# Kernel optimization log

Measured on AMD Instinct MI355X. Metric: run time of the kernel, lower is better.

The kernel has to match this reference:

```python
import jax, jax.numpy as jnp
import numpy as np

LRELU_SLOPE = 0.2
SQRT2 = 1.4142135623730951

def make_coord(h, w):
    # LIIF make_coord: cell-center coords in [-1, 1]; index 0 is the row (dim -2) coord.
    ys = -1.0 + (2.0 * jnp.arange(h, dtype=jnp.float32) + 1.0) / h
    xs = -1.0 + (2.0 * jnp.arange(w, dtype=jnp.float32) + 1.0) / w
    yy, xx = jnp.meshgrid(ys, xs, indexing='ij')
    return jnp.stack([yy, xx], axis=-1).reshape(h * w, 2)  # [Q, 2]

def style_layer(x, style_vec, scale2, shift, mod_w, mod_b, conv_w, act_b):
    # StyleGAN2-style modulated 3x3 conv + instance norm + (scale2, shift) affine + fused leaky relu.
    s = style_vec @ mod_w.T + mod_b                                   # [B, Cin] modulation
    w = conv_w[None] * s[:, None, :, None, None]                      # [B, Cout, Cin, 3, 3]
    demod = jax.lax.rsqrt(jnp.sum(w * w, axis=(2, 3, 4)) + 1e-8)      # [B, Cout]
    y = jax.lax.conv_general_dilated(x * s[:, :, None, None], conv_w, (1, 1), 'SAME',
                                     dimension_numbers=('NCHW', 'OIHW', 'NCHW'))
    y = y * demod[:, :, None, None]
    mu = jnp.mean(y, axis=(2, 3), keepdims=True)
    var = jnp.var(y, axis=(2, 3), keepdims=True)
    y = (y - mu) * jax.lax.rsqrt(var + 1e-5)                          # InstanceNorm2d (no affine)
    y = y * scale2 + shift
    return jax.nn.leaky_relu(y + act_b[None, :, None, None], LRELU_SLOPE) * SQRT2

def reference(x, scale1, scale2, shift, mod_w, mod_b, conv_w, act_b, w1, b1, w2, b2, out_h, out_w):
    B, C, Hf, Wf = x.shape
    feat = style_layer(x, scale1, scale2, shift, mod_w, mod_b, conv_w, act_b)
    Q = out_h * out_w
    coord = jnp.broadcast_to(make_coord(out_h, out_w)[None], (B, Q, 2))  # [B, Q, 2]
    rx = 1.0 / Hf  # = 2/Hf/2
    ry = 1.0 / Wf
    eps_shift = 1e-6
    feat_flat = feat.reshape(B, C, Hf * Wf).transpose(0, 2, 1)  # [B, Hf*Wf, C]
    preds, areas = [], []
    for vx in (-1, 1):
        for vy in (-1, 1):
            cy = jnp.clip(coord[..., 0] + vx * rx + eps_shift, -1.0 + 1e-6, 1.0 - 1e-6)
            cx = jnp.clip(coord[..., 1] + vy * ry + eps_shift, -1.0 + 1e-6, 1.0 - 1e-6)
            # nearest grid_sample (align_corners=False): idx = floor((c+1)/2 * size)
            iy = jnp.clip(jnp.floor((cy + 1.0) * 0.5 * Hf), 0, Hf - 1).astype(jnp.int32)
            ix = jnp.clip(jnp.floor((cx + 1.0) * 0.5 * Wf), 0, Wf - 1).astype(jnp.int32)
            lin = iy * Wf + ix                                        # [B, Q]
            q_feat = jnp.take_along_axis(feat_flat, lin[..., None], axis=1)  # [B, Q, C]
            qy = -1.0 + (2.0 * iy.astype(jnp.float32) + 1.0) / Hf     # nearest feat-cell coord
            qx = -1.0 + (2.0 * ix.astype(jnp.float32) + 1.0) / Wf
            rel_y = (coord[..., 0] - qy) * Hf
            rel_x = (coord[..., 1] - qx) * Wf
            inp = jnp.concatenate([q_feat, rel_y[..., None], rel_x[..., None]], axis=-1)  # [B,Q,C+2]
            pred = (inp @ w1 + b1) @ w2 + b2                          # two stacked Linears, no act
            preds.append(pred)
            areas.append(jnp.abs(rel_y * rel_x) + 1e-9)
    tot_area = areas[0] + areas[1] + areas[2] + areas[3]
    areas = [areas[3], areas[2], areas[1], areas[0]]  # diagonal swap (local ensemble)
    ret = jnp.zeros_like(preds[0])
    for pred, area in zip(preds, areas):
        ret = ret + pred * (area / tot_area)[..., None]
    return ret  # [B, Q, dim]

def setup_inputs() -> dict:
    key = jax.random.key(0)
    ks = jax.random.split(key, 12)
    B, C, Hf, Wf, S = 4, 64, 64, 64, 512
    return {
        'x': jax.random.normal(ks[0], (B, C, Hf, Wf), jnp.float32),
        'scale1': jax.random.normal(ks[1], (B, S), jnp.float32),
        'scale2': jax.random.normal(ks[2], (B, C, 1, 1), jnp.float32),
        'shift': jax.random.normal(ks[3], (B, C, 1, 1), jnp.float32),
        'mod_w': jax.random.normal(ks[4], (C, S), jnp.float32) * 0.02,
        'mod_b': jnp.ones((C,), jnp.float32),
        'conv_w': jax.random.normal(ks[5], (C, C, 3, 3), jnp.float32) * 0.05,
        'act_b': jax.random.normal(ks[6], (C,), jnp.float32) * 0.02,
        'w1': jax.random.normal(ks[7], (C + 2, 256), jnp.float32) * 0.05,
        'b1': jax.random.normal(ks[8], (256,), jnp.float32) * 0.01,
        'w2': jax.random.normal(ks[9], (256, C), jnp.float32) * 0.05,
        'b2': jax.random.normal(ks[10], (C,), jnp.float32) * 0.01,
        'out_h': 256,
        'out_w': 256,
    }
```

## Files before the change

kernel.cpp:

```cpp
#include <hip/hip_runtime.h>

#define SQRT2F 1.41421356237309515f

typedef __attribute__((ext_vector_type(8))) short bf16x8;
typedef __attribute__((ext_vector_type(4))) float f32x4;

enum : int {
  DM_OFF   = 0,
  BC_OFF   = 256,
  WC_OFF   = 1024,
  P_OFF    = 8192,
  Y_OFF    = 65536,
  WS_FLOATS = Y_OFF + 1048576
};

__device__ __align__(16) float WS[WS_FLOATS];
__device__ __align__(256) unsigned bar_cnt[4 * 64];
__device__ __align__(256) unsigned bar_gen[4 * 64];

__device__ __forceinline__ unsigned ld_llcu(const unsigned* p) {
  unsigned v;
  asm volatile("global_load_dword %0, %1, off sc0 sc1\n\ts_waitcnt vmcnt(0)"
               : "=v"(v) : "v"(p) : "memory");
  return v;
}
__device__ __forceinline__ float ld_llcf(const float* p) {
  float v;
  asm volatile("global_load_dword %0, %1, off sc0 sc1\n\ts_waitcnt vmcnt(0)"
               : "=v"(v) : "v"(p) : "memory");
  return v;
}
__device__ __forceinline__ f32x4 ld_llc4(const float* p) {
  f32x4 v;
  asm volatile("global_load_dwordx4 %0, %1, off sc0 sc1\n\ts_waitcnt vmcnt(0)"
               : "=v"(v) : "v"(p) : "memory");
  return v;
}
__device__ __forceinline__ void stg_llc1(float* p, float v) {
  asm volatile("global_store_dword %0, %1, off sc0 sc1"
               :: "v"(p), "v"(v) : "memory");
}
__device__ __forceinline__ void stg_llc4(float* p, f32x4 v) {
  asm volatile("global_store_dwordx4 %0, %1, off sc0 sc1"
               :: "v"(p), "v"(v) : "memory");
}

struct ConvSh {
  unsigned short Xl[3 * 66 * 64];
  unsigned short Wl[64 * 24 * 8];
  float part[512];
  float s_sh[64];
};
struct GoutSh {
  unsigned short ftb[128][72];
  unsigned short WcTb[64][72];
  float G[100][68];
  float red[2048];
  float A[64], B[64], bcl[64];
};
union ShU { ConvSh c; GoutSh g; };

__device__ __forceinline__ unsigned short f2bf(float v) {
  unsigned int u = __float_as_uint(v);
  u += 0x7fffu + ((u >> 16) & 1u);
  return (unsigned short)(u >> 16);
}

__global__ __launch_bounds__(512) void mega_kernel(
    const float* __restrict__ x,      const float* __restrict__ scale1,
    const float* __restrict__ scale2, const float* __restrict__ shiftp,
    const float* __restrict__ mod_w,  const float* __restrict__ mod_b,
    const float* __restrict__ conv_w, const float* __restrict__ act_b,
    const float* __restrict__ b1,     const float* __restrict__ w2,
    const float* __restrict__ b2,     const float* __restrict__ w1,
    float* __restrict__ out) {
  const int bid = blockIdx.x;
  const int b = bid >> 6;
  const int r = bid & 63;
  const int t = threadIdx.x;
  const int w = t >> 6, lane = t & 63;
  const int l15 = lane & 15, l4 = lane >> 4;

  __shared__ __align__(16) ShU sh;

  {
    const int i = t >> 3, qq = t & 7;
    const float* sv = scale1 + b * 512 + qq * 64;
    const float* mw = mod_w + i * 512 + qq * 64;
    float p = 0.f;
    for (int k = 0; k < 64; ++k) p = fmaf(sv[k], mw[k], p);
    sh.c.part[t] = p;
  }
  __syncthreads();
  if ((t & 7) == 0) {
    const int i = t >> 3;
    float s = mod_b[i];
    #pragma unroll
    for (int k = 0; k < 8; ++k) s += sh.c.part[t + k];
    sh.c.s_sh[i] = s;
  }
  __syncthreads();

  if (r == 0) {
    const int o = t >> 3, qq = t & 7;
    const float* cw = conv_w + o * 576 + qq * 72;
    float d = 0.f;
    #pragma unroll
    for (int ii = 0; ii < 8; ++ii) {
      const float ss = sh.c.s_sh[qq * 8 + ii];
      float wsq = 0.f;
      #pragma unroll
      for (int k = 0; k < 9; ++k) { const float wv = cw[ii * 9 + k]; wsq += wv * wv; }
      d += ss * ss * wsq;
    }
    sh.c.part[t] = d;
    __syncthreads();
    if ((t & 7) == 0) {
      float dd = 1e-8f;
      #pragma unroll
      for (int k = 0; k < 8; ++k) dd += sh.c.part[t + k];
      stg_llc1(&WS[DM_OFF + b * 64 + (t >> 3)], rsqrtf(dd));
    }
    __syncthreads();
  }

  if (r >= 1 && r <= 8) {
    const int idx = (r - 1) * 512 + t;
    const int c = idx >> 6, o = idx & 63;
    const float* r1 = w1 + c * 256;
    float a = 0.f;
    for (int k = 0; k < 256; ++k) a = fmaf(r1[k], w2[k * 64 + o], a);
    stg_llc1(&WS[WC_OFF + idx], a);
  } else if (r == 9) {
    if (t < 128) {
      const int idx = 4096 + t;
      const int c = idx >> 6, o = idx & 63;
      const float* r1 = w1 + c * 256;
      float a = 0.f;
      for (int k = 0; k < 256; ++k) a = fmaf(r1[k], w2[k * 64 + o], a);
      stg_llc1(&WS[WC_OFF + idx], a);
    } else if (t < 192) {
      const int o = t - 128;
      float a = 0.f;
      for (int k = 0; k < 256; ++k) a = fmaf(b1[k], w2[k * 64 + o], a);
      stg_llc1(&WS[BC_OFF + o], a + b2[o]);
    }
  }

  {
    int4* Xz = (int4*)sh.c.Xl;
    int4 z; z.x = z.y = z.z = z.w = 0;
    for (int idx = t; idx < 1584; idx += 512) Xz[idx] = z;
  }
  __syncthreads();

  {
    const int col = t & 63;
    const int tq = t >> 6;
    unsigned int* Xw = (unsigned int*)sh.c.Xl;
    #pragma unroll
    for (int it = 0; it < 12; ++it) {
      const int task = it * 8 + tq;
      const int row3 = task >> 5;
      const int ich = (task & 31) * 2;
      const int rr = r - 1 + row3;
      if (rr >= 0 && rr < 64) {
        const float* xb = x + ((size_t)(b * 64 + ich) << 12) + (rr << 6) + col;
        const float v0 = xb[0] * sh.c.s_sh[ich];
        const float v1 = xb[4096] * sh.c.s_sh[ich + 1];
        const unsigned int u = (unsigned int)f2bf(v0) | ((unsigned int)f2bf(v1) << 16);
        const int colp = col + 1;
        const int byte = ((row3 * 66 + colp) << 7) + ((((ich >> 3)) ^ (colp & 7)) << 4) + ((ich & 7) << 1);
        Xw[byte >> 2] = u;
      }
    }
  }

  const int oh = w >> 2, pg = w & 3;
  f32x4 acc[2];
  acc[0] = (f32x4){0.f, 0.f, 0.f, 0.f};
  acc[1] = (f32x4){0.f, 0.f, 0.f, 0.f};

  const bf16x8* Xv = (const bf16x8*)sh.c.Xl;
  const bf16x8* Wv = (const bf16x8*)sh.c.Wl;
  int4* Wst = (int4*)sh.c.Wl;

  for (int dy = 0; dy < 3; ++dy) {
    __syncthreads();
    #pragma unroll
    for (int i = 0; i < 3; ++i) {
      const int idx = i * 512 + t;
      const int o = idx / 24;
      const int g = idx - o * 24;
      const int dx = g >> 3, gg = g & 7;
      const float* cw = conv_w + o * 576 + (gg * 8) * 9 + dy * 3 + dx;
      int4 v;
      v.x = (int)((unsigned int)f2bf(cw[0])  | ((unsigned int)f2bf(cw[9])  << 16));
      v.y = (int)((unsigned int)f2bf(cw[18]) | ((unsigned int)f2bf(cw[27]) << 16));
      v.z = (int)((unsigned int)f2bf(cw[36]) | ((unsigned int)f2bf(cw[45]) << 16));
      v.w = (int)((unsigned int)f2bf(cw[54]) | ((unsigned int)f2bf(cw[63]) << 16));
      Wst[o * 24 + dx * 8 + (gg ^ (o & 7))] = v;
    }
    __syncthreads();

    #pragma unroll
    for (int dx = 0; dx < 3; ++dx) {
      #pragma unroll
      for (int kh = 0; kh < 2; ++kh) {
        const int kg = kh * 4 + l4;
        bf16x8 afr[2];
        #pragma unroll
        for (int m = 0; m < 2; ++m) {
          const int o = oh * 32 + m * 16 + l15;
          afr[m] = Wv[o * 24 + dx * 8 + (kg ^ (o & 7))];
        }
        const int colp = pg * 16 + l15 + dx;
        const bf16x8 bfr = Xv[((dy * 66 + colp) << 3) + (kg ^ (colp & 7))];
        #pragma unroll
        for (int m = 0; m < 2; ++m)
          acc[m] = __builtin_amdgcn_mfma_f32_16x16x32_bf16(
              afr[m], bfr, acc[m], 0, 0, 0);
      }
    }
  }

  {
    const int px = pg * 16 + l15;
    float* yq = WS + Y_OFF + (((size_t)b * 4096 + r * 64 + px) << 6);
    #pragma unroll
    for (int m = 0; m < 2; ++m)
      stg_llc4(yq + oh * 32 + m * 16 + l4 * 4, acc[m]);
  }

  __syncthreads();
  {
    float* sred = sh.c.part;
    #pragma unroll
    for (int m = 0; m < 2; ++m) {
      #pragma unroll
      for (int j = 0; j < 4; ++j) {
        float s1 = acc[m][j];
        float s2 = acc[m][j] * acc[m][j];
        #pragma unroll
        for (int off = 1; off < 16; off <<= 1) {
          s1 += __shfl_xor(s1, off);
          s2 += __shfl_xor(s2, off);
        }
        if (l15 == 0) {
          const int ol = m * 16 + l4 * 4 + j;
          sred[(w * 32 + ol) * 2 + 0] = s1;
          sred[(w * 32 + ol) * 2 + 1] = s2;
        }
      }
    }
    __syncthreads();
    if (t < 128) {
      const int o = t >> 1, wh = t & 1;
      const int ohh = o >> 5, ol = o & 31;
      float s = 0.f;
      #pragma unroll
      for (int pq = 0; pq < 4; ++pq)
        s += sred[(((ohh * 4 + pq) * 32) + ol) * 2 + wh];
      stg_llc1(&WS[P_OFF + (((size_t)b * 64 + r) * 64 + o) * 2 + wh], s);
    }
  }

  asm volatile("s_waitcnt vmcnt(0)" ::: "memory");
  __syncthreads();
  if (t == 0) {
    unsigned* cnt = &bar_cnt[b * 64];
    unsigned* gen = &bar_gen[b * 64];
    const unsigned g0 = ld_llcu(gen);
    const unsigned old = __hip_atomic_fetch_add(cnt, 1u, __ATOMIC_RELAXED,
                                                __HIP_MEMORY_SCOPE_AGENT);
    if (old == 63u) {
      __hip_atomic_store(cnt, 0u, __ATOMIC_RELAXED, __HIP_MEMORY_SCOPE_AGENT);
      __hip_atomic_fetch_add(gen, 1u, __ATOMIC_RELAXED,
                             __HIP_MEMORY_SCOPE_AGENT);
    } else {
      while (ld_llcu(gen) == g0) __builtin_amdgcn_s_sleep(8);
    }
  }
  __syncthreads();

  const int ty = (bid >> 3) & 7;
  const int tx = bid & 7;
  float* WcL = &sh.g.G[0][0];

  {
    f32x4 ps = (f32x4){0.f, 0.f, 0.f, 0.f};
    const float* Pb = WS + P_OFF + (size_t)b * 8192;
    #pragma unroll
    for (int k = 0; k < 4; ++k) {
      const f32x4 v = ld_llc4(Pb + (size_t)(t + k * 512) * 4);
      ps += v;
    }
    *(f32x4*)&sh.g.red[(t >> 5) * 128 + (t & 31) * 4] = ps;

    for (int i4 = t; i4 < 1072; i4 += 512) {
      const f32x4 v = (i4 < 1056) ? ld_llc4(WS + WC_OFF + i4 * 4)
                                  : ld_llc4(WS + BC_OFF + (i4 - 1056) * 4);
      *(f32x4*)&WcL[i4 * 4] = v;
    }
  }
  __syncthreads();

  const int sub = t & 3, chb = sub * 16;
  float4 wa[4], wb[4];
  #pragma unroll
  for (int k = 0; k < 4; ++k) {
    wa[k] = *(const float4*)&WcL[64 * 64 + chb + k * 4];
    wb[k] = *(const float4*)&WcL[65 * 64 + chb + k * 4];
  }
  if (t < 64) {
    float S1 = 0.f, S2 = 0.f;
    #pragma unroll
    for (int m = 0; m < 16; ++m) {
      S1 += sh.g.red[m * 128 + t * 2];
      S2 += sh.g.red[m * 128 + t * 2 + 1];
    }
    const float mu = S1 * (1.f / 4096.f);
    const float var = S2 * (1.f / 4096.f) - mu * mu;
    const float dm = ld_llcf(WS + DM_OFF + b * 64 + t);
    const float rstd = rsqrtf(dm * dm * var + 1e-5f);
    const float A = dm * rstd * scale2[b * 64 + t];
    sh.g.A[t] = A;
    sh.g.B[t] = -mu * A + shiftp[b * 64 + t] + act_b[t];
    sh.g.bcl[t] = WcL[4224 + t];
  }
  {
    const int o = t >> 3, g = t & 7;
    int4 pk;
    unsigned int e0, e1, e2, e3;
    e0 = (unsigned int)f2bf(WcL[(g * 8 + 0) * 64 + o]) |
         ((unsigned int)f2bf(WcL[(g * 8 + 1) * 64 + o]) << 16);
    e1 = (unsigned int)f2bf(WcL[(g * 8 + 2) * 64 + o]) |
         ((unsigned int)f2bf(WcL[(g * 8 + 3) * 64 + o]) << 16);
    e2 = (unsigned int)f2bf(WcL[(g * 8 + 4) * 64 + o]) |
         ((unsigned int)f2bf(WcL[(g * 8 + 5) * 64 + o]) << 16);
    e3 = (unsigned int)f2bf(WcL[(g * 8 + 6) * 64 + o]) |
         ((unsigned int)f2bf(WcL[(g * 8 + 7) * 64 + o]) << 16);
    pk.x = (int)e0; pk.y = (int)e1; pk.z = (int)e2; pk.w = (int)e3;
    *(int4*)&sh.g.WcTb[o][g * 8] = pk;
  }
  __syncthreads();

  const int cy_base = ty * 8 - 1, cx_base = tx * 8 - 1;
  {
    const float4* A4 = (const float4*)sh.g.A;
    const float4* B4 = (const float4*)sh.g.B;
    const float* yb = WS + Y_OFF + ((size_t)b << 18);
    for (int f = t; f < 1600; f += 512) {
      const int cell = f >> 4, cq = f & 15;
      const int li = cell / 10, lj = cell - li * 10;
      const int ciy = cy_base + li, cix = cx_base + lj;
      if (ciy >= 0 && ciy < 64 && cix >= 0 && cix < 64) {
        const f32x4 y4 = ld_llc4(yb + (((size_t)(ciy << 6) + cix) << 6) + cq * 4);
        const float4 Av = A4[cq], Bv = B4[cq];
        float f0, f1, f2, f3, u;
        u = y4[0] * Av.x + Bv.x; f0 = (u > 0.f ? u : 0.2f * u) * SQRT2F;
        u = y4[1] * Av.y + Bv.y; f1 = (u > 0.f ? u : 0.2f * u) * SQRT2F;
        u = y4[2] * Av.z + Bv.z; f2 = (u > 0.f ? u : 0.2f * u) * SQRT2F;
        u = y4[3] * Av.w + Bv.w; f3 = (u > 0.f ? u : 0.2f * u) * SQRT2F;
        uint2 u2;
        u2.x = (unsigned int)f2bf(f0) | ((unsigned int)f2bf(f1) << 16);
        u2.y = (unsigned int)f2bf(f2) | ((unsigned int)f2bf(f3) << 16);
        *(uint2*)&sh.g.ftb[cell][cq * 4] = u2;
      }
    }
  }
  __syncthreads();

  if (w < 7) {
    bf16x8 afr[2];
    #pragma unroll
    for (int kt = 0; kt < 2; ++kt)
      afr[kt] = *(const bf16x8*)&sh.g.ftb[w * 16 + l15][kt * 32 + l4 * 8];
    #pragma unroll
    for (int n = 0; n < 4; ++n) {
      const float bcv = sh.g.bcl[n * 16 + l15];
      f32x4 gacc = (f32x4){bcv, bcv, bcv, bcv};
      #pragma unroll
      for (int kt = 0; kt < 2; ++kt) {
        const bf16x8 bfr =
            *(const bf16x8*)&sh.g.WcTb[n * 16 + l15][kt * 32 + l4 * 8];
        gacc = __builtin_amdgcn_mfma_f32_16x16x32_bf16(afr[kt], bfr, gacc, 0, 0, 0);
      }
      #pragma unroll
      for (int j = 0; j < 4; ++j) {
        const int row = w * 16 + l4 * 4 + j;
        if (row < 100) sh.g.G[row][n * 16 + l15] = gacc[j];
      }
    }
  }
  __syncthreads();

  const float lo = -1.f + 1e-6f, hi = 1.f - 1e-6f;
  #pragma unroll 1
  for (int pass = 0; pass < 8; ++pass) {
    const int qi = pass * 128 + (t >> 2);
    const int oy = (ty << 5) + (qi >> 5), ox = (tx << 5) + (qi & 31);

    const float cy0 = -1.f + (2.f * oy + 1.f) * (1.f / 256.f);
    const float cx0 = -1.f + (2.f * ox + 1.f) * (1.f / 256.f);

    int lcell[4];
    float area[4], rely[4], relx[4];
    int j = 0;
    #pragma unroll
    for (int vx = -1; vx <= 1; vx += 2) {
      #pragma unroll
      for (int vy = -1; vy <= 1; vy += 2) {
        float cy = cy0 + (float)vx * (1.f / 64.f) + 1e-6f;
        cy = fminf(fmaxf(cy, lo), hi);
        float cx = cx0 + (float)vy * (1.f / 64.f) + 1e-6f;
        cx = fminf(fmaxf(cx, lo), hi);
        const float fy = floorf((cy + 1.f) * 32.f);
        const float fx = floorf((cx + 1.f) * 32.f);
        const int iy = (int)fminf(fmaxf(fy, 0.f), 63.f);
        const int ix = (int)fminf(fmaxf(fx, 0.f), 63.f);
        const float qy = -1.f + (2.f * iy + 1.f) * (1.f / 64.f);
        const float qx = -1.f + (2.f * ix + 1.f) * (1.f / 64.f);
        const float ry_ = (cy0 - qy) * 64.f;
        const float rx_ = (cx0 - qx) * 64.f;
        lcell[j] = (iy - cy_base) * 10 + (ix - cx_base);
        rely[j] = ry_; relx[j] = rx_;
        area[j] = fabsf(ry_ * rx_) + 1e-9f;
        ++j;
      }
    }
    const float tot = area[0] + area[1] + area[2] + area[3];
    float wgt[4];
    #pragma unroll
    for (int k = 0; k < 4; ++k) wgt[k] = area[3 - k] / tot;
    const float swy = wgt[0] * rely[0] + wgt[1] * rely[1] + wgt[2] * rely[2] + wgt[3] * rely[3];
    const float swx = wgt[0] * relx[0] + wgt[1] * relx[1] + wgt[2] * relx[2] + wgt[3] * relx[3];

    float4 rr[4];
    #pragma unroll
    for (int k = 0; k < 4; ++k) {
      rr[k].x = swy * wa[k].x + swx * wb[k].x;
      rr[k].y = swy * wa[k].y + swx * wb[k].y;
      rr[k].z = swy * wa[k].z + swx * wb[k].z;
      rr[k].w = swy * wa[k].w + swx * wb[k].w;
    }
    #pragma unroll
    for (int jj = 0; jj < 4; ++jj) {
      const float4* gp = (const float4*)&sh.g.G[lcell[jj]][chb];
      const float wv = wgt[jj];
      #pragma unroll
      for (int k = 0; k < 4; ++k) {
        const float4 gv = gp[k];
        rr[k].x += wv * gv.x; rr[k].y += wv * gv.y;
        rr[k].z += wv * gv.z; rr[k].w += wv * gv.w;
      }
    }
    const size_t gq = ((size_t)b << 16) + (oy << 8) + ox;
    float4* op = (float4*)(out + (gq << 6) + chb);
    #pragma unroll
    for (int k = 0; k < 4; ++k) op[k] = rr[k];
  }
}

extern "C" void kernel_launch(void* const* d_in, const int* in_sizes, int n_in,
                              void* d_out, int out_size, void* d_ws, size_t ws_size,
                              hipStream_t stream) {
  (void)in_sizes; (void)n_in; (void)out_size; (void)d_ws; (void)ws_size;
  const float* x      = (const float*)d_in[0];
  const float* scale1 = (const float*)d_in[1];
  const float* scale2 = (const float*)d_in[2];
  const float* shiftp = (const float*)d_in[3];
  const float* mod_w  = (const float*)d_in[4];
  const float* mod_b  = (const float*)d_in[5];
  const float* conv_w = (const float*)d_in[6];
  const float* act_b  = (const float*)d_in[7];
  const float* w1     = (const float*)d_in[8];
  const float* b1     = (const float*)d_in[9];
  const float* w2     = (const float*)d_in[10];
  const float* b2     = (const float*)d_in[11];
  float* out = (float*)d_out;

  hipLaunchKernelGGL(mega_kernel, dim3(256), dim3(512), 0, stream,
                     x, scale1, scale2, shiftp, mod_w, mod_b, conv_w, act_b,
                     b1, w2, b2, w1, out);
}
```

Before: 64.42 us.

## Spread weight-fold work across all blocks, batch LLC loads, use single grid barrier

Precomputing the folded MLP weight matrix (w1·w2 and b1·w2+b2) was done by eight or nine blocks with 512 threads each. It now runs on 17 threads in each of the 256 blocks after the conv, which shortens the critical path in those blocks. The per-batch barrier becomes one global barrier over all 256 blocks, since every block now needs weights that other blocks produce. After the barrier, the partial-stat, weight and feature-tile loads are all issued before a single vmcnt wait instead of waiting after each load, at the cost of more registers. The global barrier adds contention on one counter and couples all batches.

```diff
diff --git a/kernel.cpp b/kernel.cpp
--- a/kernel.cpp
+++ b/kernel.cpp
@@ -15,8 +15,8 @@
 };
 
 __device__ __align__(16) float WS[WS_FLOATS];
-__device__ __align__(256) unsigned bar_cnt[4 * 64];
-__device__ __align__(256) unsigned bar_gen[4 * 64];
+__device__ __align__(256) unsigned bar_cnt[64];
+__device__ __align__(256) unsigned bar_gen[64];
 
 __device__ __forceinline__ unsigned ld_llcu(const unsigned* p) {
   unsigned v;
@@ -30,11 +30,12 @@
                : "=v"(v) : "v"(p) : "memory");
   return v;
 }
-__device__ __forceinline__ f32x4 ld_llc4(const float* p) {
-  f32x4 v;
-  asm volatile("global_load_dwordx4 %0, %1, off sc0 sc1\n\ts_waitcnt vmcnt(0)"
+__device__ __forceinline__ void ld_llc4_nw(const float* p, f32x4& v) {
+  asm volatile("global_load_dwordx4 %0, %1, off sc0 sc1"
                : "=v"(v) : "v"(p) : "memory");
-  return v;
+}
+__device__ __forceinline__ void llc_wait() {
+  asm volatile("s_waitcnt vmcnt(0)" ::: "memory");
 }
 __device__ __forceinline__ void stg_llc1(float* p, float v) {
   asm volatile("global_store_dword %0, %1, off sc0 sc1"
@@ -124,29 +125,6 @@
     __syncthreads();
   }
 
-  if (r >= 1 && r <= 8) {
-    const int idx = (r - 1) * 512 + t;
-    const int c = idx >> 6, o = idx & 63;
-    const float* r1 = w1 + c * 256;
-    float a = 0.f;
-    for (int k = 0; k < 256; ++k) a = fmaf(r1[k], w2[k * 64 + o], a);
-    stg_llc1(&WS[WC_OFF + idx], a);
-  } else if (r == 9) {
-    if (t < 128) {
-      const int idx = 4096 + t;
-      const int c = idx >> 6, o = idx & 63;
-      const float* r1 = w1 + c * 256;
-      float a = 0.f;
-      for (int k = 0; k < 256; ++k) a = fmaf(r1[k], w2[k * 64 + o], a);
-      stg_llc1(&WS[WC_OFF + idx], a);
-    } else if (t < 192) {
-      const int o = t - 128;
-      float a = 0.f;
-      for (int k = 0; k < 256; ++k) a = fmaf(b1[k], w2[k * 64 + o], a);
-      stg_llc1(&WS[BC_OFF + o], a + b2[o]);
-    }
-  }
-
   {
     int4* Xz = (int4*)sh.c.Xl;
     int4 z; z.x = z.y = z.z = z.w = 0;
@@ -265,15 +243,31 @@
     }
   }
 
+  if (t < 17) {
+    const int idx = t * 256 + bid;
+    if (idx < 4224) {
+      const int c = idx >> 6, o = idx & 63;
+      const float* r1 = w1 + c * 256;
+      float a = 0.f;
+      for (int k = 0; k < 256; ++k) a = fmaf(r1[k], w2[k * 64 + o], a);
+      stg_llc1(&WS[WC_OFF + idx], a);
+    } else if (idx < 4288) {
+      const int o = idx - 4224;
+      float a = 0.f;
+      for (int k = 0; k < 256; ++k) a = fmaf(b1[k], w2[k * 64 + o], a);
+      stg_llc1(&WS[BC_OFF + o], a + b2[o]);
+    }
+  }
+
   asm volatile("s_waitcnt vmcnt(0)" ::: "memory");
   __syncthreads();
   if (t == 0) {
-    unsigned* cnt = &bar_cnt[b * 64];
-    unsigned* gen = &bar_gen[b * 64];
+    unsigned* cnt = &bar_cnt[0];
+    unsigned* gen = &bar_gen[0];
     const unsigned g0 = ld_llcu(gen);
     const unsigned old = __hip_atomic_fetch_add(cnt, 1u, __ATOMIC_RELAXED,
                                                 __HIP_MEMORY_SCOPE_AGENT);
-    if (old == 63u) {
+    if (old == 255u) {
       __hip_atomic_store(cnt, 0u, __ATOMIC_RELAXED, __HIP_MEMORY_SCOPE_AGENT);
       __hip_atomic_fetch_add(gen, 1u, __ATOMIC_RELAXED,
                              __HIP_MEMORY_SCOPE_AGENT);
@@ -285,23 +279,46 @@
 
   const int ty = (bid >> 3) & 7;
   const int tx = bid & 7;
+  const int cy_base = ty * 8 - 1, cx_base = tx * 8 - 1;
   float* WcL = &sh.g.G[0][0];
 
-  {
-    f32x4 ps = (f32x4){0.f, 0.f, 0.f, 0.f};
+  f32x4 pv0, pv1, pv2, pv3, wv0, wv1, wv2, yv[4];
+  int ycell[4], ycq[4];
+  bool yok[4];
+  {
     const float* Pb = WS + P_OFF + (size_t)b * 8192;
+    ld_llc4_nw(Pb + (size_t)t * 4, pv0);
+    ld_llc4_nw(Pb + (size_t)(t + 512) * 4, pv1);
+    ld_llc4_nw(Pb + (size_t)(t + 1024) * 4, pv2);
+    ld_llc4_nw(Pb + (size_t)(t + 1536) * 4, pv3);
+    ld_llc4_nw(WS + WC_OFF + (size_t)t * 4, wv0);
+    ld_llc4_nw(WS + WC_OFF + (size_t)(t + 512) * 4, wv1);
+    const int i4 = 1024 + t;
+    const float* wp2 = (i4 < 1056) ? (WS + WC_OFF + (size_t)i4 * 4)
+                     : (i4 < 1072) ? (WS + BC_OFF + (size_t)(i4 - 1056) * 4)
+                                   : (WS + WC_OFF);
+    ld_llc4_nw(wp2, wv2);
+    const float* yb = WS + Y_OFF + ((size_t)b << 18);
     #pragma unroll
     for (int k = 0; k < 4; ++k) {
-      const f32x4 v = ld_llc4(Pb + (size_t)(t + k * 512) * 4);
-      ps += v;
-    }
+      const int f = t + k * 512;
+      const int cell = f >> 4, cq = f & 15;
+      const int li = cell / 10, lj = cell - li * 10;
+      const int ciy = cy_base + li, cix = cx_base + lj;
+      const bool ok = (f < 1600) && ciy >= 0 && ciy < 64 && cix >= 0 && cix < 64;
+      ycell[k] = cell; ycq[k] = cq; yok[k] = ok;
+      const float* ya = ok ? (yb + (((size_t)(ciy << 6) + cix) << 6) + cq * 4) : yb;
+      ld_llc4_nw(ya, yv[k]);
+    }
+    llc_wait();
+  }
+
+  {
+    const f32x4 ps = pv0 + pv1 + pv2 + pv3;
     *(f32x4*)&sh.g.red[(t >> 5) * 128 + (t & 31) * 4] = ps;
-
-    for (int i4 = t; i4 < 1072; i4 += 512) {
-      const f32x4 v = (i4 < 1056) ? ld_llc4(WS + WC_OFF + i4 * 4)
-                                  : ld_llc4(WS + BC_OFF + (i4 - 1056) * 4);
-      *(f32x4*)&WcL[i4 * 4] = v;
-    }
+    *(f32x4*)&WcL[t * 4] = wv0;
+    *(f32x4*)&WcL[(t + 512) * 4] = wv1;
+    if (1024 + t < 1072) *(f32x4*)&WcL[(1024 + t) * 4] = wv2;
   }
   __syncthreads();
 
@@ -345,27 +362,22 @@
   }
   __syncthreads();
 
-  const int cy_base = ty * 8 - 1, cx_base = tx * 8 - 1;
   {
     const float4* A4 = (const float4*)sh.g.A;
     const float4* B4 = (const float4*)sh.g.B;
-    const float* yb = WS + Y_OFF + ((size_t)b << 18);
-    for (int f = t; f < 1600; f += 512) {
-      const int cell = f >> 4, cq = f & 15;
-      const int li = cell / 10, lj = cell - li * 10;
-      const int ciy = cy_base + li, cix = cx_base + lj;
-      if (ciy >= 0 && ciy < 64 && cix >= 0 && cix < 64) {
-        const f32x4 y4 = ld_llc4(yb + (((size_t)(ciy << 6) + cix) << 6) + cq * 4);
-        const float4 Av = A4[cq], Bv = B4[cq];
+    #pragma unroll
+    for (int k = 0; k < 4; ++k) {
+      if (yok[k]) {
+        const float4 Av = A4[ycq[k]], Bv = B4[ycq[k]];
         float f0, f1, f2, f3, u;
-        u = y4[0] * Av.x + Bv.x; f0 = (u > 0.f ? u : 0.2f * u) * SQRT2F;
-        u = y4[1] * Av.y + Bv.y; f1 = (u > 0.f ? u : 0.2f * u) * SQRT2F;
-        u = y4[2] * Av.z + Bv.z; f2 = (u > 0.f ? u : 0.2f * u) * SQRT2F;
-        u = y4[3] * Av.w + Bv.w; f3 = (u > 0.f ? u : 0.2f * u) * SQRT2F;
+        u = yv[k][0] * Av.x + Bv.x; f0 = (u > 0.f ? u : 0.2f * u) * SQRT2F;
+        u = yv[k][1] * Av.y + Bv.y; f1 = (u > 0.f ? u : 0.2f * u) * SQRT2F;
+        u = yv[k][2] * Av.z + Bv.z; f2 = (u > 0.f ? u : 0.2f * u) * SQRT2F;
+        u = yv[k][3] * Av.w + Bv.w; f3 = (u > 0.f ? u : 0.2f * u) * SQRT2F;
         uint2 u2;
         u2.x = (unsigned int)f2bf(f0) | ((unsigned int)f2bf(f1) << 16);
         u2.y = (unsigned int)f2bf(f2) | ((unsigned int)f2bf(f3) << 16);
-        *(uint2*)&sh.g.ftb[cell][cq * 4] = u2;
+        *(uint2*)&sh.g.ftb[ycell[k]][ycq[k] * 4] = u2;
       }
     }
   }
```

Result: slower. 68.19 us (+5.8%).
